# Performance work log

Measured on AMD Instinct MI355X. Metric: run time of the kernel, lower is better.

The kernel has to match this reference:

```python
import jax, jax.numpy as jnp
import numpy as np

B, N, S, D2, K = 16, 4096, 512, 384, 5
BIG = 1e10
EPS = float(np.finfo(np.float32).eps)


def masked_bn(x, mask_f, gamma, beta):
    # x: [B, N, C]; mask_f: [B, N, 1] float. Training-mode batch norm over valid positions only.
    n = jnp.maximum(mask_f.sum(), 1.0)
    mean = (x * mask_f).sum(axis=(0, 1)) / n                       # [C]
    var = (jnp.square(x - mean) * mask_f).sum(axis=(0, 1)) / n     # [C]
    xh = (x - mean) * jax.lax.rsqrt(var + 1e-5)
    return (xh * gamma + beta) * mask_f


def setup_inputs() -> dict:
    key = jax.random.key(0)
    ks = jax.random.split(key, 10)
    xyz1 = jax.random.normal(ks[0], (B, N, 3), dtype=jnp.float32)
    xyz2 = jax.random.normal(ks[1], (B, S, 3), dtype=jnp.float32)
    points1 = jax.random.normal(ks[2], (B, N, 3), dtype=jnp.float32)
    points2 = jax.random.normal(ks[3], (B, S, D2), dtype=jnp.float32)
    point_lens = jax.random.randint(ks[4], (B,), N // 2, N + 1)
    embedding_lens = jax.random.randint(ks[5], (B,), S // 2, S + 1)
    point_mask = jnp.arange(N)[None, :] < point_lens[:, None]      # [B, N] bool
    W0 = jax.random.normal(ks[6], (D2, D2 + 3), dtype=jnp.float32) * 0.02
    W1 = jax.random.normal(ks[7], (D2, D2), dtype=jnp.float32) * 0.02
    return {
        "xyz1": xyz1, "xyz2": xyz2, "points1": points1, "points2": points2,
        "point_lens": point_lens, "embedding_lens": embedding_lens,
        "point_mask": point_mask,
        "W0": W0, "gamma0": jnp.ones((D2,), jnp.float32), "beta0": jnp.zeros((D2,), jnp.float32),
        "W1": W1, "gamma1": jnp.ones((D2,), jnp.float32), "beta1": jnp.zeros((D2,), jnp.float32),
    }


def reference(xyz1, xyz2, points1, points2, point_lens, embedding_lens, point_mask,
              W0, gamma0, beta0, W1, gamma1, beta1):
    # --- KNN (squared euclidean, ragged key lengths) ---
    diff = xyz1[:, :, None, :] - xyz2[:, None, :, :]               # [B, N, S, 3]
    d2 = jnp.sum(diff * diff, axis=-1)                             # [B, N, S]
    key_valid = jnp.arange(S)[None, :] < embedding_lens[:, None]   # [B, S]
    d2 = jnp.where(key_valid[:, None, :], d2, BIG)
    neg_d, idx = jax.lax.top_k(-d2, K)                             # [B, N, K]
    dists = -neg_d

    # --- inverse-distance weighted interpolation ---
    dist_recip = 1.0 / (dists + EPS)
    weight = dist_recip / dist_recip.sum(axis=2, keepdims=True)    # [B, N, K]
    gathered = jax.vmap(lambda p, i: p[i])(points2, idx)           # [B, N, K, D2]
    interpolated = (gathered * weight[..., None]).sum(axis=2)      # [B, N, D2]

    # --- concat coords + MLP (1x1 conv, masked BN, GELU) ---
    new_points = jnp.concatenate([points1, interpolated], axis=-1)  # [B, N, D2+3]
    mask_f = point_mask[..., None].astype(new_points.dtype)

    x = jnp.einsum('bnc,oc->bno', new_points, W0)
    x = masked_bn(x, mask_f, gamma0, beta0)
    x = jax.nn.gelu(x, approximate=False)
    x = jnp.einsum('bnc,oc->bno', x, W1)
    x = masked_bn(x, mask_f, gamma1, beta1)
    return x, idx
```

## Files before the change

kernel.cpp:

```cpp
#include <hip/hip_runtime.h>
#include <stdint.h>

typedef unsigned short u16;
typedef unsigned int u32;

#define B_ 16
#define N_ 4096
#define S_ 512
#define D2_ 384
#define K_ 5
#define CIN 387
#define KP 416
#define M_ (B_*N_)

typedef float f32x4 __attribute__((ext_vector_type(4)));
typedef u32 u32x4 __attribute__((ext_vector_type(4)));
typedef __bf16 bf16x8 __attribute__((ext_vector_type(8)));

__device__ __forceinline__ float bf2f(u16 h) {
  union { u32 u; float f; } v; v.u = ((u32)h) << 16; return v.f;
}
__device__ __forceinline__ u16 f2bf(float f) {
  union { float f; u32 u; } v; v.f = f;
  u32 u = v.u;
  u32 r = (u + 0x7FFFu + ((u >> 16) & 1u)) >> 16;
  return (u16)r;
}

__device__ __forceinline__ float erf_approx(float x) {
  float ax = fabsf(x);
  float t = __builtin_amdgcn_rcpf(fmaf(0.3275911f, ax, 1.0f));
  float p = fmaf(t, 1.061405429f, -1.453152027f);
  p = fmaf(p, t, 1.421413741f);
  p = fmaf(p, t, -0.284496736f);
  p = fmaf(p, t, 0.254829592f);
  p = p * t;
  float e = __expf(-ax * ax);
  float r = fmaf(-p, e, 1.0f);
  return copysignf(r, x);
}

__device__ __forceinline__ float gelu_f(float y) {
  return 0.5f * y * (1.f + erf_approx(y * 0.70710678118654752f));
}

__device__ __forceinline__ void gld16(const void* g, void* l) {
  __builtin_amdgcn_global_load_lds(
      (const __attribute__((address_space(1))) unsigned int*)g,
      (__attribute__((address_space(3))) unsigned int*)l, 16, 0, 0);
}

__global__ void zero_kernel(float* __restrict__ p, int nel) {
  int i = blockIdx.x * 256 + threadIdx.x;
  if (i < nel) p[i] = 0.f;
}

__global__ void pad_w0_kernel(const float* __restrict__ W0, u16* __restrict__ W0p) {
  int i = blockIdx.x * 256 + threadIdx.x;
  int r = i / KP, c = i - r * KP;
  W0p[i] = (c < CIN) ? f2bf(W0[r * CIN + c]) : (u16)0;
}

__global__ void conv_w1_kernel(const float* __restrict__ W1, u16* __restrict__ W1c) {
  int i = blockIdx.x * 256 + threadIdx.x;
  W1c[i] = f2bf(W1[i]);
}

__global__ __launch_bounds__(256) void knn_kernel(
    const float* __restrict__ xyz1, const float* __restrict__ xyz2,
    const float* __restrict__ points1, const int* __restrict__ emb_lens,
    u16* __restrict__ A1, float* __restrict__ idx_out,
    float* __restrict__ wq, int* __restrict__ iq)
{
  __shared__ float4 sxyz[S_];
  __shared__ float sd[256][K_];
  __shared__ int   si[256][K_];

  int b = blockIdx.x >> 5;
  int n0 = (blockIdx.x & 31) << 7;
  int tid = threadIdx.x;

  const float* kb = xyz2 + (size_t)b * S_ * 3;
  for (int i = tid; i < S_; i += 256)
    sxyz[i] = make_float4(kb[3*i], kb[3*i+1], kb[3*i+2], 0.f);
  __syncthreads();

  int L = emb_lens[b];
  int q = tid & 127, chunk = tid >> 7;
  const float* qp = xyz1 + ((size_t)b * N_ + n0 + q) * 3;
  float qx = qp[0], qy = qp[1], qz = qp[2];

  float d0=3e38f, d1=3e38f, d2=3e38f, d3=3e38f, d4=3e38f;
  int   i0=0, i1=0, i2=0, i3=0, i4=0;
  int sbase = chunk << 8;
  #pragma unroll 4
  for (int t = 0; t < 256; ++t) {
    int s = sbase + t;
    float4 k4 = sxyz[s];
    float dx = __fsub_rn(qx, k4.x), dy = __fsub_rn(qy, k4.y), dz = __fsub_rn(qz, k4.z);
    float dd = __fadd_rn(__fadd_rn(__fmul_rn(dx,dx), __fmul_rn(dy,dy)),
                         __fmul_rn(dz,dz));
    if (s >= L) dd = 1e10f;
    if (dd < d4) {
      if (dd < d3) { d4=d3; i4=i3;
        if (dd < d2) { d3=d2; i3=i2;
          if (dd < d1) { d2=d1; i2=i1;
            if (dd < d0) { d1=d0; i1=i0; d0=dd; i0=s; }
            else         { d1=dd; i1=s; }
          } else { d2=dd; i2=s; }
        } else { d3=dd; i3=s; }
      } else { d4=dd; i4=s; }
    }
  }
  sd[tid][0]=d0; sd[tid][1]=d1; sd[tid][2]=d2; sd[tid][3]=d3; sd[tid][4]=d4;
  si[tid][0]=i0; si[tid][1]=i1; si[tid][2]=i2; si[tid][3]=i3; si[tid][4]=i4;
  __syncthreads();

  if (tid < 128) {
    float md[K_]; int mi[K_];
    int pa = 0, pb = 0;
    #pragma unroll
    for (int k = 0; k < K_; ++k) {
      float da_ = sd[tid][pa], db_ = sd[tid + 128][pb];
      bool ta = da_ <= db_;
      md[k] = ta ? da_ : db_;
      mi[k] = ta ? si[tid][pa] : si[tid + 128][pb];
      pa += ta ? 1 : 0; pb += ta ? 0 : 1;
    }
    float w[K_]; float ws = 0.f;
    #pragma unroll
    for (int k = 0; k < K_; ++k) { w[k] = 1.f / (md[k] + 1.1920929e-7f); ws += w[k]; }
    float inv = 1.f / ws;
    size_t row = (size_t)b * N_ + n0 + tid;
    #pragma unroll
    for (int k = 0; k < K_; ++k) {
      wq[row * K_ + k] = w[k] * inv;
      iq[row * K_ + k] = mi[k];
      idx_out[row * K_ + k] = (float)mi[k];
    }
    u16* rp = A1 + row * KP;
    const float* p1 = points1 + row * 3;
    rp[0] = f2bf(p1[0]); rp[1] = f2bf(p1[1]); rp[2] = f2bf(p1[2]);
    #pragma unroll
    for (int c = CIN; c < KP; ++c) rp[c] = 0;
  }
}

__global__ __launch_bounds__(256) void interp_kernel(
    const float* __restrict__ points2,
    const float* __restrict__ wq, const int* __restrict__ iq,
    u16* __restrict__ A1)
{
  int lane = threadIdx.x & 63, wid = threadIdx.x >> 6;
  int i = blockIdx.x;
  int gq = ((i & 7) << 13) + ((i >> 3) << 2) + wid;
  int b = gq >> 12;

  float w[K_]; int id[K_];
  #pragma unroll
  for (int k = 0; k < K_; ++k) {
    w[k] = wq[(size_t)gq * K_ + k];
    id[k] = iq[(size_t)gq * K_ + k];
  }
  const float* p2 = points2 + (size_t)b * S_ * D2_;
  const float* r0 = p2 + (size_t)id[0] * D2_;
  const float* r1 = p2 + (size_t)id[1] * D2_;
  const float* r2 = p2 + (size_t)id[2] * D2_;
  const float* r3 = p2 + (size_t)id[3] * D2_;
  const float* r4 = p2 + (size_t)id[4] * D2_;
  u16* rp = A1 + (size_t)gq * KP + 3;
  #pragma unroll
  for (int j = 0; j < 6; ++j) {
    int c = j * 64 + lane;
    float acc = w[0]*r0[c] + w[1]*r1[c] + w[2]*r2[c] + w[3]*r3[c] + w[4]*r4[c];
    rp[c] = f2bf(acc);
  }
}

template<bool F32OUT>
__global__ __launch_bounds__(256) void gemm_nt_kernel(
    const u16* __restrict__ A, int lda,
    const u16* __restrict__ W, int ldw,
    void* __restrict__ Cv, int ldc, int KT,
    const int* __restrict__ lens, float* __restrict__ sums)
{
  __shared__ __align__(16) u16 sA[2][128 * 32];
  __shared__ __align__(16) u16 sB[2][128 * 32];
  __shared__ float lsum[128], lsq[128];
  int tid = threadIdx.x;
  int lane = tid & 63, wid = tid >> 6;
  u32 bi = blockIdx.x;
  u32 s = bi >> 3;
  int m0 = (int)(((bi & 7) * 64 + s / 3) * 128);
  int n0 = (int)((s % 3) * 128);
  int wm = (wid & 1) * 64, wn = (wid >> 1) * 64;
  int frow = lane & 15, quad = lane >> 4;

  if (tid < 128) { lsum[tid] = 0.f; lsq[tid] = 0.f; }

  int grow = wid * 16 + (lane >> 2);
  int cq = (lane & 3) * 8;
  const u16* gA0 = A + (size_t)(m0 + grow) * lda + cq;
  const u16* gA1 = gA0 + (size_t)64 * lda;
  const u16* gB0 = W + (size_t)(n0 + grow) * ldw + cq;
  const u16* gB1 = gB0 + (size_t)64 * ldw;

  f32x4 acc[4][4];
  f32x4 zero4 = {0.f, 0.f, 0.f, 0.f};
  #pragma unroll
  for (int i = 0; i < 4; ++i)
    #pragma unroll
    for (int j = 0; j < 4; ++j) acc[i][j] = zero4;

  gld16(gA0, sA[0] + wid * 512); gld16(gA1, sA[0] + (wid + 4) * 512);
  gld16(gB0, sB[0] + wid * 512); gld16(gB1, sB[0] + (wid + 4) * 512);
  gA0 += 32; gA1 += 32; gB0 += 32; gB1 += 32;

  for (int kt = 0; kt < KT; ++kt) {
    __syncthreads();
    int p = kt & 1;
    if (kt + 1 < KT) {
      int np = p ^ 1;
      gld16(gA0, sA[np] + wid * 512); gld16(gA1, sA[np] + (wid + 4) * 512);
      gld16(gB0, sB[np] + wid * 512); gld16(gB1, sB[np] + (wid + 4) * 512);
      gA0 += 32; gA1 += 32; gB0 += 32; gB1 += 32;
    }
    bf16x8 af[4], bfr[4];
    #pragma unroll
    for (int i = 0; i < 4; ++i)
      af[i] = *(const bf16x8*)(sA[p] + (wm + i * 16 + frow) * 32 + quad * 8);
    #pragma unroll
    for (int j = 0; j < 4; ++j)
      bfr[j] = *(const bf16x8*)(sB[p] + (wn + j * 16 + frow) * 32 + quad * 8);
    #pragma unroll
    for (int i = 0; i < 4; ++i)
      #pragma unroll
      for (int j = 0; j < 4; ++j)
        acc[i][j] = __builtin_amdgcn_mfma_f32_16x16x32_bf16(af[i], bfr[j], acc[i][j], 0, 0, 0);
  }

  int len = lens[m0 >> 12];
  float colS[4] = {0,0,0,0}, colQ[4] = {0,0,0,0};
  #pragma unroll
  for (int i = 0; i < 4; ++i) {
    #pragma unroll
    for (int j = 0; j < 4; ++j) {
      int col = n0 + wn + j * 16 + frow;
      #pragma unroll
      for (int r = 0; r < 4; ++r) {
        int m = m0 + wm + i * 16 + quad * 4 + r;
        float v = acc[i][j][r];
        if constexpr (F32OUT) ((float*)Cv)[(size_t)m * ldc + col] = v;
        else                  ((u16*)Cv)[(size_t)m * ldc + col] = f2bf(v);
        float x = ((m & 4095) < len) ? v : 0.f;
        colS[j] += x; colQ[j] += x * x;
      }
    }
  }
  #pragma unroll
  for (int j = 0; j < 4; ++j) {
    colS[j] += __shfl_xor(colS[j], 16); colS[j] += __shfl_xor(colS[j], 32);
    colQ[j] += __shfl_xor(colQ[j], 16); colQ[j] += __shfl_xor(colQ[j], 32);
    if (lane < 16) {
      int cl = wn + j * 16 + frow;
      atomicAdd(&lsum[cl], colS[j]);
      atomicAdd(&lsq[cl], colQ[j]);
    }
  }
  __syncthreads();
  if (tid < 128) {
    atomicAdd(&sums[n0 + tid], lsum[tid]);
    atomicAdd(&sums[384 + n0 + tid], lsq[tid]);
  }
}

__global__ void bn_finalize_kernel(const float* __restrict__ sums,
    const float* __restrict__ gamma, const float* __restrict__ beta,
    const int* __restrict__ lens, float* __restrict__ par)
{
  int c = threadIdx.x;
  float nv = 0.f;
  for (int b = 0; b < B_; ++b) nv += (float)lens[b];
  float mean = sums[c] / nv;
  float var = sums[384 + c] / nv - mean * mean;
  var = fmaxf(var, 0.f);
  float rstd = rsqrtf(var + 1e-5f);
  float a = rstd * gamma[c];
  par[c] = a;
  par[384 + c] = beta[c] - mean * a;
}

__global__ __launch_bounds__(256) void apply_bn_gelu_kernel(
    u16* __restrict__ X, const float* __restrict__ par)
{
  int t = blockIdx.x * 256 + threadIdx.x;
  int r0 = t / 48;
  int c0 = (t - r0 * 48) * 8;
  f32x4 pa0 = *(const f32x4*)(par + c0);
  f32x4 pa1 = *(const f32x4*)(par + c0 + 4);
  f32x4 pb0 = *(const f32x4*)(par + 384 + c0);
  f32x4 pb1 = *(const f32x4*)(par + 384 + c0 + 4);
  float a[8]  = {pa0[0], pa0[1], pa0[2], pa0[3], pa1[0], pa1[1], pa1[2], pa1[3]};
  float bb[8] = {pb0[0], pb0[1], pb0[2], pb0[3], pb1[0], pb1[1], pb1[2], pb1[3]};
  u16* base = X + (size_t)r0 * D2_ + c0;
  const size_t rstride = (size_t)4096 * D2_;

  #pragma unroll
  for (int g = 0; g < 2; ++g) {
    u32x4 v[8];
    #pragma unroll
    for (int it = 0; it < 8; ++it)
      v[it] = *(const u32x4*)(base + (size_t)(g * 8 + it) * rstride);
    #pragma unroll
    for (int it = 0; it < 8; ++it) {
      const u16* h = (const u16*)&v[it];
      u32x4 o; u16* ho = (u16*)&o;
      #pragma unroll
      for (int j = 0; j < 8; ++j) {
        float y = fmaf(bf2f(h[j]), a[j], bb[j]);
        ho[j] = f2bf(gelu_f(y));
      }
      *(u32x4*)(base + (size_t)(g * 8 + it) * rstride) = o;
    }
  }
}

__global__ __launch_bounds__(256) void apply_bn_out_kernel(
    const u16* __restrict__ X, const float* __restrict__ par,
    const int* __restrict__ lens, float* __restrict__ out)
{
  int t = blockIdx.x * 256 + threadIdx.x;
  int r0 = t / 48;
  int c0 = (t - r0 * 48) * 8;
  f32x4 pa0 = *(const f32x4*)(par + c0);
  f32x4 pa1 = *(const f32x4*)(par + c0 + 4);
  f32x4 pb0 = *(const f32x4*)(par + 384 + c0);
  f32x4 pb1 = *(const f32x4*)(par + 384 + c0 + 4);
  float a[8]  = {pa0[0], pa0[1], pa0[2], pa0[3], pa1[0], pa1[1], pa1[2], pa1[3]};
  float bb[8] = {pb0[0], pb0[1], pb0[2], pb0[3], pb1[0], pb1[1], pb1[2], pb1[3]};
  const u16* src = X + (size_t)r0 * D2_ + c0;
  float* dst = out + (size_t)r0 * D2_ + c0;
  const size_t rstride = (size_t)4096 * D2_;

  #pragma unroll
  for (int g = 0; g < 2; ++g) {
    u32x4 v[8];
    #pragma unroll
    for (int it = 0; it < 8; ++it)
      v[it] = *(const u32x4*)(src + (size_t)(g * 8 + it) * rstride);
    #pragma unroll
    for (int it = 0; it < 8; ++it) {
      int b = g * 8 + it;
      bool valid = r0 < lens[b];
      const u16* h = (const u16*)&v[it];
      f32x4 o0, o1;
      #pragma unroll
      for (int j = 0; j < 4; ++j) {
        float y = fmaf(bf2f(h[j]), a[j], bb[j]);
        o0[j] = valid ? y : 0.f;
      }
      #pragma unroll
      for (int j = 0; j < 4; ++j) {
        float y = fmaf(bf2f(h[4 + j]), a[4 + j], bb[4 + j]);
        o1[j] = valid ? y : 0.f;
      }
      float* op = dst + (size_t)b * rstride;
      __builtin_nontemporal_store(o0, (f32x4*)op);
      __builtin_nontemporal_store(o1, (f32x4*)(op + 4));
    }
  }
}

extern "C" void kernel_launch(void* const* d_in, const int* in_sizes, int n_in,
                              void* d_out, int out_size, void* d_ws, size_t ws_size,
                              hipStream_t stream) {
  const float* xyz1    = (const float*)d_in[0];
  const float* xyz2    = (const float*)d_in[1];
  const float* points1 = (const float*)d_in[2];
  const float* points2 = (const float*)d_in[3];
  const int* point_lens = (const int*)d_in[4];
  const int* emb_lens   = (const int*)d_in[5];
  const float* W0 = (const float*)d_in[7];
  const float* g0 = (const float*)d_in[8];
  const float* b0 = (const float*)d_in[9];
  const float* W1 = (const float*)d_in[10];
  const float* g1 = (const float*)d_in[11];
  const float* b1 = (const float*)d_in[12];

  float* out = (float*)d_out;
  float* idx_out = out + (size_t)M_ * D2_;

  char* w = (char*)d_ws;
  u16* A1    = (u16*)w;
  u16* x1    = (u16*)w;
  u16* W0p   = (u16*)(w + 54525952);
  u16* W1c   = (u16*)(w + 54845440);
  u16* x0    = (u16*)(w + 55140352);
  float* wq  = (float*)(w + 55140352);
  int*   iq  = (int*)(w + 56451072);
  float* stats = (float*)(w + 105472000);
  float* par   = (float*)(w + 105478144);

  zero_kernel<<<6, 256, 0, stream>>>(stats, 1536);
  pad_w0_kernel<<<624, 256, 0, stream>>>(W0, W0p);
  conv_w1_kernel<<<576, 256, 0, stream>>>(W1, W1c);
  knn_kernel<<<512, 256, 0, stream>>>(xyz1, xyz2, points1, emb_lens,
                                      A1, idx_out, wq, iq);
  interp_kernel<<<16384, 256, 0, stream>>>(points2, wq, iq, A1);
  gemm_nt_kernel<false><<<1536, 256, 0, stream>>>(
      A1, KP, W0p, KP, x0, D2_, 13, point_lens, stats);
  bn_finalize_kernel<<<1, 384, 0, stream>>>(stats, g0, b0, point_lens, par);
  apply_bn_gelu_kernel<<<768, 256, 0, stream>>>(x0, par);
  gemm_nt_kernel<false><<<1536, 256, 0, stream>>>(
      x0, D2_, W1c, D2_, x1, D2_, 12, point_lens, stats + 768);
  bn_finalize_kernel<<<1, 384, 0, stream>>>(stats + 768, g1, b1, point_lens, par + 768);
  apply_bn_out_kernel<<<768, 256, 0, stream>>>(x1, par + 768, point_lens, out);
}
```

Measured before the change: 344.5 us.

## Triple-buffer GEMM shared tiles with explicit vmcnt waits and compile-time K loop

```diff
diff --git a/kernel.cpp b/kernel.cpp
--- a/kernel.cpp
+++ b/kernel.cpp
@@ -177,15 +177,15 @@
   }
 }
 
-template<bool F32OUT>
+template<bool F32OUT, int KT>
 __global__ __launch_bounds__(256) void gemm_nt_kernel(
     const u16* __restrict__ A, int lda,
     const u16* __restrict__ W, int ldw,
-    void* __restrict__ Cv, int ldc, int KT,
+    void* __restrict__ Cv, int ldc,
     const int* __restrict__ lens, float* __restrict__ sums)
 {
-  __shared__ __align__(16) u16 sA[2][128 * 32];
-  __shared__ __align__(16) u16 sB[2][128 * 32];
+  __shared__ __align__(16) u16 sA[3][128 * 32];
+  __shared__ __align__(16) u16 sB[3][128 * 32];
   __shared__ float lsum[128], lsq[128];
   int tid = threadIdx.x;
   int lane = tid & 63, wid = tid >> 6;
@@ -212,26 +212,30 @@
     #pragma unroll
     for (int j = 0; j < 4; ++j) acc[i][j] = zero4;
 
-  gld16(gA0, sA[0] + wid * 512); gld16(gA1, sA[0] + (wid + 4) * 512);
-  gld16(gB0, sB[0] + wid * 512); gld16(gB1, sB[0] + (wid + 4) * 512);
-  gA0 += 32; gA1 += 32; gB0 += 32; gB1 += 32;
-
+  auto stage = [&](int buf) {
+    gld16(gA0, sA[buf] + wid * 512); gld16(gA1, sA[buf] + (wid + 4) * 512);
+    gld16(gB0, sB[buf] + wid * 512); gld16(gB1, sB[buf] + (wid + 4) * 512);
+    gA0 += 32; gA1 += 32; gB0 += 32; gB1 += 32;
+  };
+
+  stage(0); stage(1);
+
+  #pragma unroll
   for (int kt = 0; kt < KT; ++kt) {
-    __syncthreads();
-    int p = kt & 1;
-    if (kt + 1 < KT) {
-      int np = p ^ 1;
-      gld16(gA0, sA[np] + wid * 512); gld16(gA1, sA[np] + (wid + 4) * 512);
-      gld16(gB0, sB[np] + wid * 512); gld16(gB1, sB[np] + (wid + 4) * 512);
-      gA0 += 32; gA1 += 32; gB0 += 32; gB1 += 32;
-    }
+    if (kt + 1 < KT) asm volatile("s_waitcnt vmcnt(4)" ::: "memory");
+    else             asm volatile("s_waitcnt vmcnt(0)" ::: "memory");
+    __builtin_amdgcn_s_barrier();
+    if (kt + 2 < KT) stage((kt + 2) % 3);
+
+    const u16* pA = sA[kt % 3];
+    const u16* pB = sB[kt % 3];
     bf16x8 af[4], bfr[4];
     #pragma unroll
     for (int i = 0; i < 4; ++i)
-      af[i] = *(const bf16x8*)(sA[p] + (wm + i * 16 + frow) * 32 + quad * 8);
+      af[i] = *(const bf16x8*)(pA + (wm + i * 16 + frow) * 32 + quad * 8);
     #pragma unroll
     for (int j = 0; j < 4; ++j)
-      bfr[j] = *(const bf16x8*)(sB[p] + (wn + j * 16 + frow) * 32 + quad * 8);
+      bfr[j] = *(const bf16x8*)(pB + (wn + j * 16 + frow) * 32 + quad * 8);
     #pragma unroll
     for (int i = 0; i < 4; ++i)
       #pragma unroll
@@ -407,12 +411,12 @@
   knn_kernel<<<512, 256, 0, stream>>>(xyz1, xyz2, points1, emb_lens,
                                       A1, idx_out, wq, iq);
   interp_kernel<<<16384, 256, 0, stream>>>(points2, wq, iq, A1);
-  gemm_nt_kernel<false><<<1536, 256, 0, stream>>>(
-      A1, KP, W0p, KP, x0, D2_, 13, point_lens, stats);
+  gemm_nt_kernel<false, 13><<<1536, 256, 0, stream>>>(
+      A1, KP, W0p, KP, x0, D2_, point_lens, stats);
   bn_finalize_kernel<<<1, 384, 0, stream>>>(stats, g0, b0, point_lens, par);
   apply_bn_gelu_kernel<<<768, 256, 0, stream>>>(x0, par);
-  gemm_nt_kernel<false><<<1536, 256, 0, stream>>>(
-      x0, D2_, W1c, D2_, x1, D2_, 12, point_lens, stats + 768);
+  gemm_nt_kernel<false, 12><<<1536, 256, 0, stream>>>(
+      x0, D2_, W1c, D2_, x1, D2_, point_lens, stats + 768);
   bn_finalize_kernel<<<1, 384, 0, stream>>>(stats + 768, g1, b1, point_lens, par + 768);
   apply_bn_out_kernel<<<768, 256, 0, stream>>>(x1, par + 768, point_lens, out);
 }
```

Result: no change. 342.2 us (-0.7%).
